# Kernel tuning notes

Measured on AMD Instinct MI355X. Metric: run time of the kernel, lower is better.

The kernel has to match this reference:

```python
import jax, jax.numpy as jnp
import numpy as np

B, S, HID = 2, 2048, 2048
N_HEADS, N_KV = 16, 8
HEAD_DIM = HID // N_HEADS  # 128
N_REP = N_HEADS // N_KV


def setup_inputs() -> dict:
    key = jax.random.key(0)
    ks = jax.random.split(key, 5)
    x = jax.random.normal(ks[0], (B, S, HID), dtype=jnp.float32)
    Wq = jax.random.normal(ks[1], (HID, N_HEADS * HEAD_DIM), dtype=jnp.float32) * 0.02
    Wk = jax.random.normal(ks[2], (HID, N_KV * HEAD_DIM), dtype=jnp.float32) * 0.02
    Wv = jax.random.normal(ks[3], (HID, N_KV * HEAD_DIM), dtype=jnp.float32) * 0.02
    Wo = jax.random.normal(ks[4], (N_HEADS * HEAD_DIM, HID), dtype=jnp.float32) * 0.02
    # standard RoPE frequencies: theta_i = 10000^(-2i/head_dim), angle = pos * theta_i
    inv_freq = 1.0 / (10000.0 ** (jnp.arange(0, HEAD_DIM, 2, dtype=jnp.float32) / HEAD_DIM))
    angles = jnp.arange(S, dtype=jnp.float32)[:, None] * inv_freq[None, :]  # [S, HEAD_DIM/2]
    return {
        "x": x, "Wq": Wq, "Wk": Wk, "Wv": Wv, "Wo": Wo,
        "freqs_cos": jnp.cos(angles), "freqs_sin": jnp.sin(angles),
        "start_pos": 0,
    }


def _rope(t, cos, sin):
    # t: [B, S, h, head_dim]; complex-view pairs are (even, odd) along last dim
    tr = t.reshape(*t.shape[:-1], -1, 2)
    re, im = tr[..., 0], tr[..., 1]
    cos = cos[None, :, None, :]
    sin = sin[None, :, None, :]
    out_re = re * cos - im * sin
    out_im = re * sin + im * cos
    return jnp.stack([out_re, out_im], axis=-1).reshape(t.shape)


def reference(x, Wq, Wk, Wv, Wo, freqs_cos, freqs_sin, start_pos):
    b, s, _ = x.shape
    xq = (x @ Wq).reshape(b, s, N_HEADS, HEAD_DIM)
    xk = (x @ Wk).reshape(b, s, N_KV, HEAD_DIM)
    xv = (x @ Wv).reshape(b, s, N_KV, HEAD_DIM)
    xq = _rope(xq, freqs_cos, freqs_sin)
    xk = _rope(xk, freqs_cos, freqs_sin)
    # repeat_kv: each kv head duplicated n_rep times consecutively
    xk = jnp.repeat(xk, N_REP, axis=2)  # [b, s, N_HEADS, hd]
    xv = jnp.repeat(xv, N_REP, axis=2)
    scale = 1.0 / jnp.sqrt(jnp.float32(HEAD_DIM))
    attn = jnp.einsum("bqhd,bkhd->bhqk", xq, xk) * scale
    attn = jax.nn.softmax(attn, axis=-1)
    out = jnp.einsum("bhqk,bkhd->bqhd", attn, xv).reshape(b, s, N_HEADS * HEAD_DIM)
    return out @ Wo
```

## Files before the change

kernel.cpp:

```cpp
#include <hip/hip_runtime.h>
#include <stdint.h>

#define DI __device__ __forceinline__

typedef unsigned short u16;
typedef unsigned int   u32;
typedef __attribute__((ext_vector_type(8))) short short8;
typedef __attribute__((ext_vector_type(4))) float f32x4;


DI u16 f2bf(float f) {
    u32 u = __float_as_uint(f);
    u32 r = u + 0x7fff + ((u >> 16) & 1);
    return (u16)(r >> 16);
}
DI u32 pk2bf(float a, float b) {
    return (u32)f2bf(a) | ((u32)f2bf(b) << 16);
}
DI float bf2f(u16 h) { return __uint_as_float(((u32)h) << 16); }

DI f32x4 mfma16(short8 a, short8 b, f32x4 c) {
    return __builtin_amdgcn_mfma_f32_16x16x32_bf16(a, b, c, 0, 0, 0);
}

DI void gload_lds16(const void* g, void* l) {
    __builtin_amdgcn_global_load_lds(
        (const __attribute__((address_space(1))) void*)g,
        (__attribute__((address_space(3))) void*)l, 16, 0, 0);
}

DI short8 rope8(short8 raw, const float* cp, const float* sp, float osc) {
    float4 c4 = *(const float4*)cp;
    float4 s4 = *(const float4*)sp;
    u32* rp = (u32*)&raw;
#pragma unroll
    for (int p = 0; p < 4; p++) {
        u32 v = rp[p];
        float re = __uint_as_float(v << 16);
        float im = __uint_as_float(v & 0xffff0000u);
        float cc = ((const float*)&c4)[p] * osc;
        float ss = ((const float*)&s4)[p] * osc;
        rp[p] = pk2bf(re * cc - im * ss, re * ss + im * cc);
    }
    return raw;
}

__global__ __launch_bounds__(256) void cvt_x(const float* __restrict__ x,
                                             u16* __restrict__ o, int n4) {
    int i = blockIdx.x * 256 + threadIdx.x;
    if (i >= n4) return;
    float4 v = *(const float4*)(x + (size_t)i * 4);
    uint2 p; p.x = pk2bf(v.x, v.y); p.y = pk2bf(v.z, v.w);
    *(uint2*)(o + (size_t)i * 4) = p;
}

__global__ __launch_bounds__(256) void transpose_cvt4(const float* __restrict__ W0,
                                                      const float* __restrict__ W1,
                                                      const float* __restrict__ W2,
                                                      const float* __restrict__ W3,
                                                      u16* __restrict__ D0,
                                                      u16* __restrict__ D1,
                                                      u16* __restrict__ D2,
                                                      u16* __restrict__ D3) {
    const float* W; u16* D; int N;
    switch (blockIdx.z) {
        case 0:  W = W0; D = D0; N = 2048; break;
        case 1:  W = W1; D = D1; N = 1024; break;
        case 2:  W = W2; D = D2; N = 1024; break;
        default: W = W3; D = D3; N = 2048; break;
    }
    if ((int)blockIdx.x >= (N >> 6)) return;
    const int K = 2048;
    __shared__ u16 tl[64][65];
    int tx = threadIdx.x & 15, ty = threadIdx.x >> 4;
    int tc = blockIdx.x * 64, tr = blockIdx.y * 64;
#pragma unroll
    for (int i = 0; i < 4; i++) {
        int r = tr + ty + i * 16;
        float4 v = *(const float4*)&W[(size_t)r * N + tc + tx * 4];
        tl[tx*4+0][ty+i*16] = f2bf(v.x);
        tl[tx*4+1][ty+i*16] = f2bf(v.y);
        tl[tx*4+2][ty+i*16] = f2bf(v.z);
        tl[tx*4+3][ty+i*16] = f2bf(v.w);
    }
    __syncthreads();
#pragma unroll
    for (int i = 0; i < 4; i++) {
        int n = tc + ty + i * 16;
        uint2 p;
        p.x = (u32)tl[ty+i*16][tx*4+0] | ((u32)tl[ty+i*16][tx*4+1] << 16);
        p.y = (u32)tl[ty+i*16][tx*4+2] | ((u32)tl[ty+i*16][tx*4+3] << 16);
        *(uint2*)&D[(size_t)n * K + tr + tx * 4] = p;
    }
}

__global__ __launch_bounds__(256) void rope_kernel(u16* __restrict__ buf,
                                                   const float* __restrict__ fc,
                                                   const float* __restrict__ fs,
                                                   int H, int tokshift, int total,
                                                   float oscale) {
    int idx = blockIdx.x * 256 + threadIdx.x;
    if (idx >= total) return;
    int tok = idx >> tokshift;
    int rem = idx & ((1 << tokshift) - 1);
    int h = rem >> 6, j = rem & 63;
    int s = tok & 2047;
    size_t a = ((size_t)tok * H + h) * 128 + 2 * j;
    u32 v = *(u32*)(buf + a);
    float re = bf2f((u16)(v & 0xffff));
    float im = bf2f((u16)(v >> 16));
    float c = fc[s * 64 + j], sn = fs[s * 64 + j];
    *(u32*)(buf + a) = pk2bf((re * c - im * sn) * oscale,
                             (re * sn + im * c) * oscale);
}

__global__ __launch_bounds__(512) void gemm_qkv8(const u16* __restrict__ A,
                                                 const u16* __restrict__ BT,
                                                 u16* __restrict__ Qo,
                                                 u16* __restrict__ Ko,
                                                 u16* __restrict__ Vo) {
    __shared__ __align__(16) u16 SM[65536];
    char* smb = (char*)SM;
    const int tid = threadIdx.x;
    const int w = tid >> 6, l = tid & 63;
    const int l15 = l & 15, lh = l >> 4;
    const int wr = w >> 2, wc = w & 3;

    const int bid = blockIdx.x;
    const int sw = (bid & 7) * 32 + (bid >> 3);
    const int bx = sw & 15, by = sw >> 4;

    const char* Ag = (const char*)A  + (size_t)(by * 256) * 4096;
    const char* Bg = (const char*)BT + (size_t)(bx * 256) * 4096;

    const int r0 = tid >> 3;
    const int c0 = ((tid & 7) << 4) ^ (((tid >> 5) & 1) << 5);
    const int wb = w << 10;

#define STG_A(tt, bb, hh) do {                                              \
        const char* s_ = Ag + (size_t)((hh) * 128 + r0) * 4096 + (tt) * 128 + c0; \
        char* d_ = smb + (bb) * 65536 + (hh) * 16384 + wb;                  \
        gload_lds16(s_, d_);                                                \
        gload_lds16(s_ + (size_t)64 * 4096, d_ + 8192);                     \
    } while (0)
#define STG_B(tt, bb, hh) do {                                              \
        const char* s_ = Bg + (size_t)((hh) * 128 + r0) * 4096 + (tt) * 128 + c0; \
        char* d_ = smb + (bb) * 65536 + 32768 + (hh) * 16384 + wb;          \
        gload_lds16(s_, d_);                                                \
        gload_lds16(s_ + (size_t)64 * 4096, d_ + 8192);                     \
    } while (0)

    const int aoff = l15 * 128 + ((lh * 16) ^ (((l15 >> 2) & 1) << 5));

    const f32x4 fz = {0.f, 0.f, 0.f, 0.f};
    f32x4 acc[8][4];
#pragma unroll
    for (int m = 0; m < 8; m++)
#pragma unroll
        for (int n = 0; n < 4; n++) acc[m][n] = fz;

    STG_A(0, 0, 0); STG_A(0, 0, 1); STG_B(0, 0, 0); STG_B(0, 0, 1);
    STG_A(1, 1, 0);
    asm volatile("s_waitcnt vmcnt(2)" ::: "memory");
    __builtin_amdgcn_s_barrier();

    for (int t = 0; t < 32; ++t) {
        const int cur = t & 1;
        const int t1 = t + 1 < 32 ? t + 1 : 31;
        const int t2 = t + 2 < 32 ? t + 2 : 31;
        const char* Ab = smb + cur * 65536 + wr * 16384 + aoff;
        const char* Bb = smb + cur * 65536 + 32768 + (wc >> 1) * 16384
                         + (wc & 1) * 8192 + aoff;
        short8 aF[4][2], bF[4][2];

        STG_A(t1, cur ^ 1, 1);
#pragma unroll
        for (int m = 0; m < 4; m++) {
            aF[m][0] = *(const short8*)(Ab + m * 2048);
            aF[m][1] = *(const short8*)(Ab + m * 2048 + 64);
        }
#pragma unroll
        for (int n = 0; n < 2; n++) {
            bF[n][0] = *(const short8*)(Bb + n * 2048);
            bF[n][1] = *(const short8*)(Bb + n * 2048 + 64);
        }
        __builtin_amdgcn_s_setprio(1);
#pragma unroll
        for (int m = 0; m < 4; m++)
#pragma unroll
            for (int n = 0; n < 2; n++) {
                acc[m][n] = mfma16(aF[m][0], bF[n][0], acc[m][n]);
                acc[m][n] = mfma16(aF[m][1], bF[n][1], acc[m][n]);
            }
        __builtin_amdgcn_s_setprio(0);
        __builtin_amdgcn_s_barrier();

        STG_B(t1, cur ^ 1, 0);
#pragma unroll
        for (int n = 2; n < 4; n++) {
            bF[n][0] = *(const short8*)(Bb + n * 2048);
            bF[n][1] = *(const short8*)(Bb + n * 2048 + 64);
        }
        __builtin_amdgcn_s_setprio(1);
#pragma unroll
        for (int m = 0; m < 4; m++)
#pragma unroll
            for (int n = 2; n < 4; n++) {
                acc[m][n] = mfma16(aF[m][0], bF[n][0], acc[m][n]);
                acc[m][n] = mfma16(aF[m][1], bF[n][1], acc[m][n]);
            }
        __builtin_amdgcn_s_setprio(0);
        __builtin_amdgcn_s_barrier();

        STG_B(t1, cur ^ 1, 1);
#pragma unroll
        for (int m = 0; m < 4; m++) {
            aF[m][0] = *(const short8*)(Ab + (m + 4) * 2048);
            aF[m][1] = *(const short8*)(Ab + (m + 4) * 2048 + 64);
        }
        __builtin_amdgcn_s_setprio(1);
#pragma unroll
        for (int m = 0; m < 4; m++)
#pragma unroll
            for (int n = 0; n < 2; n++) {
                acc[m + 4][n] = mfma16(aF[m][0], bF[n][0], acc[m + 4][n]);
                acc[m + 4][n] = mfma16(aF[m][1], bF[n][1], acc[m + 4][n]);
            }
        __builtin_amdgcn_s_setprio(0);
        __builtin_amdgcn_s_barrier();

        STG_A(t2, cur, 0);
        __builtin_amdgcn_s_setprio(1);
#pragma unroll
        for (int m = 0; m < 4; m++)
#pragma unroll
            for (int n = 2; n < 4; n++) {
                acc[m + 4][n] = mfma16(aF[m][0], bF[n][0], acc[m + 4][n]);
                acc[m + 4][n] = mfma16(aF[m][1], bF[n][1], acc[m + 4][n]);
            }
        __builtin_amdgcn_s_setprio(0);
        asm volatile("s_waitcnt vmcnt(2)" ::: "memory");
        __builtin_amdgcn_s_barrier();
    }
#undef STG_A
#undef STG_B

    const int rbase = by * 256 + wr * 128 + lh * 4;
    const int cbase = bx * 256 + wc * 64 + l15;
    if (bx < 8) {
#pragma unroll
        for (int m = 0; m < 8; m++)
#pragma unroll
            for (int j = 0; j < 4; j++) {
                size_t ro = (size_t)(rbase + m * 16 + j) * 2048 + cbase;
#pragma unroll
                for (int n = 0; n < 4; n++)
                    Qo[ro + n * 16] = f2bf(acc[m][n][j]);
            }
    } else if (bx < 12) {
        const int ck = cbase - 2048;
#pragma unroll
        for (int m = 0; m < 8; m++)
#pragma unroll
            for (int j = 0; j < 4; j++) {
                size_t ro = (size_t)(rbase + m * 16 + j) * 1024 + ck;
#pragma unroll
                for (int n = 0; n < 4; n++)
                    Ko[ro + n * 16] = f2bf(acc[m][n][j]);
            }
    } else {
#pragma unroll
        for (int m = 0; m < 8; m++)
#pragma unroll
            for (int n = 0; n < 4; n++) {
                int tok = rbase + m * 16;
                int c = cbase + n * 16 - 3072;
                int bb2 = tok >> 11, ss = tok & 2047;
                int h2 = c >> 7, d = c & 127;
                uint2 v;
                v.x = pk2bf(acc[m][n][0], acc[m][n][1]);
                v.y = pk2bf(acc[m][n][2], acc[m][n][3]);
                *(uint2*)(Vo + (size_t)((bb2 * 8 + h2) * 128 + d) * 2048 + ss) = v;
            }
    }
}

__global__ __launch_bounds__(256) void gemm_wo(const u16* __restrict__ A,
                                               const u16* __restrict__ BT,
                                               float* __restrict__ Of,
                                               int M, int N, int K) {
    __shared__ u16 As[128 * 32];
    __shared__ u16 Bs[128 * 32];
    const int tid = threadIdx.x;
    const int w = tid >> 6, l = tid & 63;
    const int m0 = blockIdx.y * 128, n0 = blockIdx.x * 128;
    const int wr = w >> 1, wc = w & 1;
    const int l15 = l & 15, lh = l >> 4;

    const f32x4 fz = {0.f, 0.f, 0.f, 0.f};
    f32x4 acc[4][4];
#pragma unroll
    for (int m = 0; m < 4; m++)
#pragma unroll
        for (int n = 0; n < 4; n++) acc[m][n] = fz;

    const int rowA = w * 32 + (l >> 2);
    const int colb = (l & 3) * 8;

    for (int k0 = 0; k0 < K; k0 += 32) {
        __syncthreads();
#pragma unroll
        for (int c = 0; c < 2; c++) {
            gload_lds16(A  + (size_t)(m0 + rowA + c * 16) * K + k0 + colb,
                        &As[w * 1024 + c * 512]);
            gload_lds16(BT + (size_t)(n0 + rowA + c * 16) * K + k0 + colb,
                        &Bs[w * 1024 + c * 512]);
        }
        __syncthreads();
        short8 af[4], bfr[4];
#pragma unroll
        for (int m = 0; m < 4; m++)
            af[m] = *(const short8*)&As[(wr * 64 + m * 16 + l15) * 32 + lh * 8];
#pragma unroll
        for (int n = 0; n < 4; n++)
            bfr[n] = *(const short8*)&Bs[(wc * 64 + n * 16 + l15) * 32 + lh * 8];
#pragma unroll
        for (int m = 0; m < 4; m++)
#pragma unroll
            for (int n = 0; n < 4; n++)
                acc[m][n] = mfma16(af[m], bfr[n], acc[m][n]);
    }

    const int rbase = m0 + wr * 64 + lh * 4;
    const int cbase = n0 + wc * 64 + l15;
#pragma unroll
    for (int m = 0; m < 4; m++)
#pragma unroll
        for (int j = 0; j < 4; j++) {
            size_t ro = (size_t)(rbase + m * 16 + j) * N + cbase;
#pragma unroll
            for (int n = 0; n < 4; n++)
                Of[ro + n * 16] = acc[m][n][j];
        }
}

__global__ __launch_bounds__(256, 2) void attn_kernel(const u16* __restrict__ Q,
                                                      const u16* __restrict__ Kg,
                                                      const u16* __restrict__ Vg,
                                                      const float* __restrict__ fc,
                                                      const float* __restrict__ fs,
                                                      u16* __restrict__ O) {
    __shared__ __align__(16) u16 Ks[2][8192];
    __shared__ __align__(16) u16 Vs[2][8192];
    __shared__ __align__(16) u16 Ps[4][2048];
    const int tid = threadIdx.x;
    const int w = tid >> 6, l = tid & 63;
    const int qt = blockIdx.x, bh = blockIdx.y;
    const int b = bh >> 4, h = bh & 15, h2 = h >> 1;
    const int l15 = l & 15, lh = l >> 4;

    char* KsB = (char*)&Ks[0][0];
    char* VsB = (char*)&Vs[0][0];
    char* PsB = (char*)&Ps[w][0];

    const char* Kbase = (const char*)Kg + (size_t)b * 2048 * 2048 + h2 * 256;
    const char* Vbase = (const char*)Vg + (size_t)(b * 8 + h2) * 128 * 4096;
    int krow[4], kcol[4], vrow[4], vcol[4];
#pragma unroll
    for (int c = 0; c < 4; c++) {
        int X = c * 4096 + tid * 16;
        krow[c] = X >> 8; kcol[c] = (X & 255) ^ ((krow[c] & 7) << 4);
        vrow[c] = X >> 7; vcol[c] = (X & 127) ^ ((vrow[c] & 7) << 4);
    }

#define STAGE(t, pb) do {                                               \
        const char* Kt = Kbase + (size_t)(t) * 131072;                  \
        const char* Vt = Vbase + (t) * 128;                             \
        char* kd = KsB + (pb) * 16384 + tid * 16;                       \
        char* vd = VsB + (pb) * 16384 + tid * 16;                       \
        _Pragma("unroll")                                               \
        for (int c = 0; c < 4; c++) {                                   \
            gload_lds16(Kt + krow[c] * 2048 + kcol[c], kd + c * 4096);  \
            gload_lds16(Vt + (size_t)vrow[c] * 4096 + vcol[c], vd + c * 4096); \
        }                                                               \
    } while (0)

    const float OSC = 0.12751742987f;
    short8 qf0[4], qf1[4];
    {
        const int s0r = qt * 128 + w * 32 + l15;
        const int s1r = s0r + 16;
        const u16* qp0 = Q + ((size_t)(b * 2048 + s0r)) * 2048 + h * 128 + lh * 8;
        const u16* qp1 = Q + ((size_t)(b * 2048 + s1r)) * 2048 + h * 128 + lh * 8;
#pragma unroll
        for (int ks = 0; ks < 4; ks++) {
            qf0[ks] = rope8(*(const short8*)(qp0 + ks * 32),
                            &fc[s0r * 64 + ks * 16 + lh * 4],
                            &fs[s0r * 64 + ks * 16 + lh * 4], OSC);
            qf1[ks] = rope8(*(const short8*)(qp1 + ks * 32),
                            &fc[s1r * 64 + ks * 16 + lh * 4],
                            &fs[s1r * 64 + ks * 16 + lh * 4], OSC);
        }
    }

    const f32x4 fz = {0.f, 0.f, 0.f, 0.f};
    f32x4 o0[8], o1[8];
#pragma unroll
    for (int n = 0; n < 8; n++) { o0[n] = fz; o1[n] = fz; }
    float mrow0[4] = {-1e30f, -1e30f, -1e30f, -1e30f};
    float mrow1[4] = {-1e30f, -1e30f, -1e30f, -1e30f};
    float lsum0[4] = {0.f, 0.f, 0.f, 0.f};
    float lsum1[4] = {0.f, 0.f, 0.f, 0.f};

    STAGE(0, 0);

    for (int t = 0; t < 32; t++) {
        __syncthreads();
        const int pb = t & 1;
        if (t < 31) STAGE(t + 1, pb ^ 1);
        const char* kc = KsB + pb * 16384;
        const char* vc = VsB + pb * 16384;
        const int swz = (l15 & 7) << 4;

        f32x4 s0[4], s1[4];
#pragma unroll
        for (int ct = 0; ct < 4; ct++) {
            s0[ct] = fz; s1[ct] = fz;
#pragma unroll
            for (int ks = 0; ks < 4; ks++) {
                short8 kf = *(const short8*)(kc + ((ct * 16 + l15) << 8)
                                                + ((ks * 64 + lh * 16) ^ swz));
                s0[ct] = mfma16(qf0[ks], kf, s0[ct]);
                s1[ct] = mfma16(qf1[ks], kf, s1[ct]);
            }
        }

        float pl0[4], pl1[4];
#pragma unroll
        for (int r = 0; r < 4; r++) {
            pl0[r] = fmaxf(fmaxf(s0[0][r], s0[1][r]), fmaxf(s0[2][r], s0[3][r]));
            pl1[r] = fmaxf(fmaxf(s1[0][r], s1[1][r]), fmaxf(s1[2][r], s1[3][r]));
        }
        bool grow = false;
#pragma unroll
        for (int r = 0; r < 4; r++)
            grow = grow || (pl0[r] > mrow0[r] + 8.f) || (pl1[r] > mrow1[r] + 8.f);
        if (__any(grow)) {
#pragma unroll
            for (int r = 0; r < 4; r++) {
                float mx = pl0[r];
                mx = fmaxf(mx, __shfl_xor(mx, 1));
                mx = fmaxf(mx, __shfl_xor(mx, 2));
                mx = fmaxf(mx, __shfl_xor(mx, 4));
                mx = fmaxf(mx, __shfl_xor(mx, 8));
                float mnew = fmaxf(mrow0[r], mx);
                float fsc = exp2f(mrow0[r] - mnew);
                mrow0[r] = mnew;
                lsum0[r] *= fsc;
#pragma unroll
                for (int n = 0; n < 8; n++) o0[n][r] *= fsc;
            }
#pragma unroll
            for (int r = 0; r < 4; r++) {
                float mx = pl1[r];
                mx = fmaxf(mx, __shfl_xor(mx, 1));
                mx = fmaxf(mx, __shfl_xor(mx, 2));
                mx = fmaxf(mx, __shfl_xor(mx, 4));
                mx = fmaxf(mx, __shfl_xor(mx, 8));
                float mnew = fmaxf(mrow1[r], mx);
                float fsc = exp2f(mrow1[r] - mnew);
                mrow1[r] = mnew;
                lsum1[r] *= fsc;
#pragma unroll
                for (int n = 0; n < 8; n++) o1[n][r] *= fsc;
            }
        }
        const int cb2 = l15 << 1;
#pragma unroll
        for (int r = 0; r < 4; r++) {
            float p0 = exp2f(s0[0][r] - mrow0[r]);
            float p1 = exp2f(s0[1][r] - mrow0[r]);
            float p2 = exp2f(s0[2][r] - mrow0[r]);
            float p3 = exp2f(s0[3][r] - mrow0[r]);
            lsum0[r] += (p0 + p1) + (p2 + p3);
            const int rw = lh * 4 + r;
            const int rb = rw << 7;
            const int sw2 = (rw & 7) << 4;
            *(u16*)(PsB + (rb + (( 0 + cb2) ^ sw2))) =
                (u16)((__float_as_uint(p0) + 0x8000u) >> 16);
            *(u16*)(PsB + (rb + ((32 + cb2) ^ sw2))) =
                (u16)((__float_as_uint(p1) + 0x8000u) >> 16);
            *(u16*)(PsB + (rb + ((64 + cb2) ^ sw2))) =
                (u16)((__float_as_uint(p2) + 0x8000u) >> 16);
            *(u16*)(PsB + (rb + ((96 + cb2) ^ sw2))) =
                (u16)((__float_as_uint(p3) + 0x8000u) >> 16);
        }
#pragma unroll
        for (int r = 0; r < 4; r++) {
            float p0 = exp2f(s1[0][r] - mrow1[r]);
            float p1 = exp2f(s1[1][r] - mrow1[r]);
            float p2 = exp2f(s1[2][r] - mrow1[r]);
            float p3 = exp2f(s1[3][r] - mrow1[r]);
            lsum1[r] += (p0 + p1) + (p2 + p3);
            const int rw = 16 + lh * 4 + r;
            const int rb = rw << 7;
            const int sw2 = (rw & 7) << 4;
            *(u16*)(PsB + (rb + (( 0 + cb2) ^ sw2))) =
                (u16)((__float_as_uint(p0) + 0x8000u) >> 16);
            *(u16*)(PsB + (rb + ((32 + cb2) ^ sw2))) =
                (u16)((__float_as_uint(p1) + 0x8000u) >> 16);
            *(u16*)(PsB + (rb + ((64 + cb2) ^ sw2))) =
                (u16)((__float_as_uint(p2) + 0x8000u) >> 16);
            *(u16*)(PsB + (rb + ((96 + cb2) ^ sw2))) =
                (u16)((__float_as_uint(p3) + 0x8000u) >> 16);
        }

#pragma unroll
        for (int ks2 = 0; ks2 < 2; ks2++) {
            short8 pf0 = *(const short8*)(PsB + ((l15 << 7)
                                + ((ks2 * 64 + lh * 16) ^ swz)));
            short8 pf1 = *(const short8*)(PsB + (((16 + l15) << 7)
                                + ((ks2 * 64 + lh * 16) ^ swz)));
#pragma unroll
            for (int n = 0; n < 8; n++) {
                short8 vf = *(const short8*)(vc + (((n * 16 + l15) << 7)
                                                  + ((ks2 * 64 + lh * 16) ^ swz)));
                o0[n] = mfma16(pf0, vf, o0[n]);
                o1[n] = mfma16(pf1, vf, o1[n]);
            }
        }
    }

    const int q0 = qt * 128 + w * 32;
    const size_t ob0 = ((size_t)(b * 2048 + q0 + lh * 4)) * 2048 + h * 128 + l15;
#pragma unroll
    for (int r = 0; r < 4; r++) {
        float ls = lsum0[r];
        ls += __shfl_xor(ls, 1);
        ls += __shfl_xor(ls, 2);
        ls += __shfl_xor(ls, 4);
        ls += __shfl_xor(ls, 8);
        float li = 1.0f / ls;
#pragma unroll
        for (int n = 0; n < 8; n++)
            O[ob0 + (size_t)r * 2048 + n * 16] = f2bf(o0[n][r] * li);
    }
    const size_t ob1 = ob0 + (size_t)16 * 2048;
#pragma unroll
    for (int r = 0; r < 4; r++) {
        float ls = lsum1[r];
        ls += __shfl_xor(ls, 1);
        ls += __shfl_xor(ls, 2);
        ls += __shfl_xor(ls, 4);
        ls += __shfl_xor(ls, 8);
        float li = 1.0f / ls;
#pragma unroll
        for (int n = 0; n < 8; n++)
            O[ob1 + (size_t)r * 2048 + n * 16] = f2bf(o1[n][r] * li);
    }
#undef STAGE
}

extern "C" void kernel_launch(void* const* d_in, const int* in_sizes, int n_in,
                              void* d_out, int out_size, void* d_ws, size_t ws_size,
                              hipStream_t stream) {
    const float* x  = (const float*)d_in[0];
    const float* Wq = (const float*)d_in[1];
    const float* Wk = (const float*)d_in[2];
    const float* Wv = (const float*)d_in[3];
    const float* Wo = (const float*)d_in[4];
    const float* fc = (const float*)d_in[5];
    const float* fs = (const float*)d_in[6];
    float* out = (float*)d_out;

    uint8_t* ws = (uint8_t*)d_ws;
    u16* xb   = (u16*)(ws + 0);
    u16* wqkv = (u16*)(ws + 16777216);
    u16* wqT  = (u16*)(ws + 16777216);
    u16* wkT  = (u16*)(ws + 25165824);
    u16* wvT  = (u16*)(ws + 29360128);
    u16* woT  = (u16*)(ws + 33554432);
    u16* qb   = (u16*)(ws + 41943040);
    u16* kb   = (u16*)(ws + 58720256);
    u16* vT   = (u16*)(ws + 67108864);
    u16* ao   = xb;

    cvt_x<<<dim3(8192), dim3(256), 0, stream>>>(x, xb, 2097152);
    transpose_cvt4<<<dim3(32, 32, 4), dim3(256), 0, stream>>>(Wq, Wk, Wv, Wo,
                                                              wqT, wkT, wvT, woT);

    gemm_qkv8<<<dim3(256), dim3(512), 0, stream>>>(xb, wqkv, qb, kb, vT);

    rope_kernel<<<dim3(8192), dim3(256), 0, stream>>>(kb, fc, fs, 8, 9, 2097152, 1.0f);

    attn_kernel<<<dim3(16, 32), dim3(256), 0, stream>>>(qb, kb, vT, fc, fs, ao);

    gemm_wo<<<dim3(16, 32), dim3(256), 0, stream>>>(ao, woT, out, 4096, 2048, 2048);
}
```

Before: 249.8 us.

## Rewrite output projection GEMM as 8-wave pipelined kernel with swizzled LDS

Replaces the simple 128x128, K=32 single-buffered Wo GEMM with a 512-thread 128x256-tile kernel. It uses BK=64, double-buffered LDS with an XOR swizzle, staggered async global-to-LDS loads split across two phases, setprio around MFMA bursts, and a grouped block-index remap for L2 locality. The aim is to hide global load latency and cut barrier stalls and LDS bank conflicts. It hardcodes the problem dimensions and uses 96KB of LDS, which limits occupancy.

```diff
diff --git a/kernel.cpp b/kernel.cpp
--- a/kernel.cpp
+++ b/kernel.cpp
@@ -285,17 +285,43 @@
     }
 }
 
-__global__ __launch_bounds__(256) void gemm_wo(const u16* __restrict__ A,
-                                               const u16* __restrict__ BT,
-                                               float* __restrict__ Of,
-                                               int M, int N, int K) {
-    __shared__ u16 As[128 * 32];
-    __shared__ u16 Bs[128 * 32];
+__global__ __launch_bounds__(512) void gemm_wo8(const u16* __restrict__ A,
+                                                const u16* __restrict__ BT,
+                                                float* __restrict__ Of) {
+    __shared__ __align__(16) u16 SM[49152];
+    char* smb = (char*)SM;
     const int tid = threadIdx.x;
     const int w = tid >> 6, l = tid & 63;
-    const int m0 = blockIdx.y * 128, n0 = blockIdx.x * 128;
-    const int wr = w >> 1, wc = w & 1;
     const int l15 = l & 15, lh = l >> 4;
+    const int wr = w >> 2, wc = w & 3;
+
+    const int bid = blockIdx.x;
+    const int sw = (bid & 7) * 32 + (bid >> 3);
+    const int bx = sw & 7, by = sw >> 3;
+
+    const char* Ag = (const char*)A  + (size_t)(by * 128) * 4096;
+    const char* Bg = (const char*)BT + (size_t)(bx * 256) * 4096;
+
+    const int r0 = tid >> 3;
+    const int c0 = ((tid & 7) << 4) ^ (((tid >> 5) & 1) << 5);
+    const int wb = w << 10;
+
+#define STG_WA(tt, bb) do {                                                 \
+        const char* s_ = Ag + (size_t)r0 * 4096 + (tt) * 128 + c0;          \
+        char* d_ = smb + (bb) * 49152 + wb;                                 \
+        gload_lds16(s_, d_);                                                \
+        gload_lds16(s_ + (size_t)64 * 4096, d_ + 8192);                     \
+    } while (0)
+#define STG_WB(tt, bb) do {                                                 \
+        const char* s_ = Bg + (size_t)r0 * 4096 + (tt) * 128 + c0;          \
+        char* d_ = smb + (bb) * 49152 + 16384 + wb;                         \
+        gload_lds16(s_, d_);                                                \
+        gload_lds16(s_ + (size_t)64 * 4096, d_ + 8192);                     \
+        gload_lds16(s_ + (size_t)128 * 4096, d_ + 16384);                   \
+        gload_lds16(s_ + (size_t)192 * 4096, d_ + 24576);                   \
+    } while (0)
+
+    const int aoff = l15 * 128 + ((lh * 16) ^ (((l15 >> 2) & 1) << 5));
 
     const f32x4 fz = {0.f, 0.f, 0.f, 0.f};
     f32x4 acc[4][4];
@@ -304,40 +330,69 @@
 #pragma unroll
         for (int n = 0; n < 4; n++) acc[m][n] = fz;
 
-    const int rowA = w * 32 + (l >> 2);
-    const int colb = (l & 3) * 8;
-
-    for (int k0 = 0; k0 < K; k0 += 32) {
-        __syncthreads();
-#pragma unroll
-        for (int c = 0; c < 2; c++) {
-            gload_lds16(A  + (size_t)(m0 + rowA + c * 16) * K + k0 + colb,
-                        &As[w * 1024 + c * 512]);
-            gload_lds16(BT + (size_t)(n0 + rowA + c * 16) * K + k0 + colb,
-                        &Bs[w * 1024 + c * 512]);
-        }
-        __syncthreads();
-        short8 af[4], bfr[4];
+    STG_WA(0, 0); STG_WB(0, 0);
+    STG_WA(1, 1);
+    asm volatile("s_waitcnt vmcnt(2)" ::: "memory");
+    __builtin_amdgcn_s_barrier();
+
+    for (int t = 0; t < 32; ++t) {
+        const int cur = t & 1;
+        const int t1 = t + 1 < 32 ? t + 1 : 31;
+        const int t2 = t + 2 < 32 ? t + 2 : 31;
+        const char* Ab = smb + cur * 49152 + wr * 8192 + aoff;
+        const char* Bb = smb + cur * 49152 + 16384 + wc * 8192 + aoff;
+        short8 aF[4][2], bF[4][2];
+
+        STG_WB(t1, cur ^ 1);
+#pragma unroll
+        for (int m = 0; m < 4; m++) {
+            aF[m][0] = *(const short8*)(Ab + m * 2048);
+            aF[m][1] = *(const short8*)(Ab + m * 2048 + 64);
+        }
+#pragma unroll
+        for (int n = 0; n < 2; n++) {
+            bF[n][0] = *(const short8*)(Bb + n * 2048);
+            bF[n][1] = *(const short8*)(Bb + n * 2048 + 64);
+        }
+        __builtin_amdgcn_s_setprio(1);
 #pragma unroll
         for (int m = 0; m < 4; m++)
-            af[m] = *(const short8*)&As[(wr * 64 + m * 16 + l15) * 32 + lh * 8];
-#pragma unroll
-        for (int n = 0; n < 4; n++)
-            bfr[n] = *(const short8*)&Bs[(wc * 64 + n * 16 + l15) * 32 + lh * 8];
+#pragma unroll
+            for (int n = 0; n < 2; n++) {
+                acc[m][n] = mfma16(aF[m][0], bF[n][0], acc[m][n]);
+                acc[m][n] = mfma16(aF[m][1], bF[n][1], acc[m][n]);
+            }
+        __builtin_amdgcn_s_setprio(0);
+        __builtin_amdgcn_s_barrier();
+
+        STG_WA(t2, cur);
+#pragma unroll
+        for (int n = 2; n < 4; n++) {
+            bF[n][0] = *(const short8*)(Bb + n * 2048);
+            bF[n][1] = *(const short8*)(Bb + n * 2048 + 64);
+        }
+        __builtin_amdgcn_s_setprio(1);
 #pragma unroll
         for (int m = 0; m < 4; m++)
 #pragma unroll
-            for (int n = 0; n < 4; n++)
-                acc[m][n] = mfma16(af[m], bfr[n], acc[m][n]);
-    }
-
-    const int rbase = m0 + wr * 64 + lh * 4;
-    const int cbase = n0 + wc * 64 + l15;
+            for (int n = 2; n < 4; n++) {
+                acc[m][n] = mfma16(aF[m][0], bF[n][0], acc[m][n]);
+                acc[m][n] = mfma16(aF[m][1], bF[n][1], acc[m][n]);
+            }
+        __builtin_amdgcn_s_setprio(0);
+        asm volatile("s_waitcnt vmcnt(2)" ::: "memory");
+        __builtin_amdgcn_s_barrier();
+    }
+#undef STG_WA
+#undef STG_WB
+
+    const int rbase = by * 128 + wr * 64 + lh * 4;
+    const int cbase = bx * 256 + wc * 64 + l15;
 #pragma unroll
     for (int m = 0; m < 4; m++)
 #pragma unroll
         for (int j = 0; j < 4; j++) {
-            size_t ro = (size_t)(rbase + m * 16 + j) * N + cbase;
+            size_t ro = (size_t)(rbase + m * 16 + j) * 2048 + cbase;
 #pragma unroll
             for (int n = 0; n < 4; n++)
                 Of[ro + n * 16] = acc[m][n][j];
@@ -595,5 +650,5 @@
 
     attn_kernel<<<dim3(16, 32), dim3(256), 0, stream>>>(qb, kb, vT, fc, fs, ao);
 
-    gemm_wo<<<dim3(16, 32), dim3(256), 0, stream>>>(ao, woT, out, 4096, 2048, 2048);
-}
+    gemm_wo8<<<dim3(256), dim3(512), 0, stream>>>(ao, woT, out);
+}
```

Result: faster. 233.3 us (-6.6%).
